# Kernel tuning notes

Measured on AMD Instinct MI355X. Metric: run time of the kernel, lower is better.

## Reference

```python
import jax, jax.numpy as jnp
import numpy as np

DEPTH, DIM, HEADS, DIM_HEAD, MLP = 6, 768, 12, 64, 3072
INNER = HEADS * DIM_HEAD  # 768
EPS = 1e-5


def _layernorm(x, w, b):
    m = jnp.mean(x, axis=-1, keepdims=True)
    v = jnp.mean((x - m) ** 2, axis=-1, keepdims=True)
    return (x - m) * jax.lax.rsqrt(v + EPS) * w + b


def setup_inputs() -> dict:
    key = jax.random.key(0)
    ks = jax.random.split(key, 12)
    s = 0.02
    return {
        "x": jax.random.normal(ks[0], (4, 1024, DIM), dtype=jnp.float32),
        "ln1_w": jnp.ones((DEPTH, DIM), jnp.float32),
        "ln1_b": jnp.zeros((DEPTH, DIM), jnp.float32),
        "w_qkv": jax.random.normal(ks[1], (DEPTH, DIM, 3 * INNER), jnp.float32) * s,
        "w_o": jax.random.normal(ks[2], (DEPTH, INNER, DIM), jnp.float32) * s,
        "b_o": jnp.zeros((DEPTH, DIM), jnp.float32),
        "ln2_w": jnp.ones((DEPTH, DIM), jnp.float32),
        "ln2_b": jnp.zeros((DEPTH, DIM), jnp.float32),
        "w1": jax.random.normal(ks[3], (DEPTH, DIM, MLP), jnp.float32) * s,
        "b1": jnp.zeros((DEPTH, MLP), jnp.float32),
        "w2": jax.random.normal(ks[4], (DEPTH, MLP, DIM), jnp.float32) * s,
        "b2": jnp.zeros((DEPTH, DIM), jnp.float32),
    }


def _forward(x, ln1_w, ln1_b, w_qkv, w_o, b_o, ln2_w, ln2_b, w1, b1, w2, b2):
    scale = DIM_HEAD ** -0.5
    b, n, _ = x.shape

    def block(x, p):
        l1w, l1b, wqkv, wo, bo, l2w, l2b, W1, B1, W2, B2 = p
        # --- attention (pre-norm); dropout/droppath are identity in eval ---
        h = _layernorm(x, l1w, l1b)
        qkv = h @ wqkv                                   # [b, n, 3*inner]
        q, k, v = jnp.split(qkv, 3, axis=-1)
        q = q.reshape(b, n, HEADS, DIM_HEAD).transpose(0, 2, 1, 3)
        k = k.reshape(b, n, HEADS, DIM_HEAD).transpose(0, 2, 1, 3)
        v = v.reshape(b, n, HEADS, DIM_HEAD).transpose(0, 2, 1, 3)
        dots = jnp.einsum('bhid,bhjd->bhij', q, k) * scale   # [b, h, n, n]
        attn = jax.nn.softmax(dots, axis=-1)
        out = jnp.einsum('bhij,bhjd->bhid', attn, v)
        out = out.transpose(0, 2, 1, 3).reshape(b, n, INNER)
        x = x + out @ wo + bo
        # --- feed-forward (pre-norm), exact GELU like torch default ---
        h = _layernorm(x, l2w, l2b)
        x = x + jax.nn.gelu(h @ W1 + B1, approximate=False) @ W2 + B2
        return x, None

    x, _ = jax.lax.scan(block, x, (ln1_w, ln1_b, w_qkv, w_o, b_o,
                                   ln2_w, ln2_b, w1, b1, w2, b2))
    return x


def reference(x, ln1_w, ln1_b, w_qkv, w_o, b_o, ln2_w, ln2_b, w1, b1, w2, b2):
    return _forward(x, ln1_w, ln1_b, w_qkv, w_o, b_o, ln2_w, ln2_b, w1, b1, w2, b2)
```

## Files before the change

### kernel.cpp

```cpp
#include <hip/hip_runtime.h>
#include <cmath>
#include <cstdint>

typedef __bf16 bf16_t;
typedef __bf16 bf16x8 __attribute__((ext_vector_type(8)));
typedef __bf16 bf16x4 __attribute__((ext_vector_type(4)));
typedef float  f32x4  __attribute__((ext_vector_type(4)));

#define DEPTH 6
#define DIM   768
#define HEADS 12
#define DH    64
#define MLPD  3072
#define SEQ   1024
#define BATCH 4
#define MTOT  (BATCH*SEQ)
#define QKVN  2304

static __device__ __forceinline__ bf16x8 ld8(const bf16_t* p) {
    return *(const bf16x8*)p;
}

typedef const __attribute__((address_space(1))) unsigned int gas_u32;
typedef __attribute__((address_space(3))) unsigned int las_u32;
static __device__ __forceinline__ void gload16(const bf16_t* g, bf16_t* l) {
    __builtin_amdgcn_global_load_lds((gas_u32*)g, (las_u32*)l, 16, 0, 0);
}

__global__ __launch_bounds__(256) void tcvt_kernel(const float* __restrict__ in,
                                                   bf16_t* __restrict__ out,
                                                   int K, int N) {
    __shared__ float ts[32][33];
    int n0 = blockIdx.x * 32, k0 = blockIdx.y * 32;
    size_t base = (size_t)blockIdx.z * K * N;
    int tx = threadIdx.x & 31, ty = threadIdx.x >> 5;
    #pragma unroll
    for (int r = 0; r < 32; r += 8)
        ts[ty + r][tx] = in[base + (size_t)(k0 + ty + r) * N + n0 + tx];
    __syncthreads();
    #pragma unroll
    for (int r = 0; r < 32; r += 8)
        out[base + (size_t)(n0 + ty + r) * K + k0 + tx] = (bf16_t)ts[tx][ty + r];
}

__global__ __launch_bounds__(192) void lnr_kernel(const float* __restrict__ xin,
                                                  float* __restrict__ xout,
                                                  const float* __restrict__ P,
                                                  int nslices,
                                                  const float* __restrict__ bias,
                                                  const float* __restrict__ w,
                                                  const float* __restrict__ b,
                                                  bf16_t* __restrict__ h,
                                                  int writeLN) {
    int row = blockIdx.x, t = threadIdx.x;
    size_t r4 = (size_t)row * 192 + t;
    float4 v = ((const float4*)xin)[r4];
    if (nslices) {
        float4 bi = ((const float4*)bias)[t];
        v.x += bi.x; v.y += bi.y; v.z += bi.z; v.w += bi.w;
        for (int s = 0; s < nslices; s++) {
            float4 pv = ((const float4*)P)[(size_t)s * MTOT * 192 + r4];
            v.x += pv.x; v.y += pv.y; v.z += pv.z; v.w += pv.w;
        }
        ((float4*)xout)[r4] = v;
    }
    float s = v.x + v.y + v.z + v.w;
    float q = v.x * v.x + v.y * v.y + v.z * v.z + v.w * v.w;
    #pragma unroll
    for (int off = 32; off > 0; off >>= 1) {
        s += __shfl_down(s, off);
        q += __shfl_down(q, off);
    }
    __shared__ float ss[3], sq[3], stat[2];
    if ((t & 63) == 0) { ss[t >> 6] = s; sq[t >> 6] = q; }
    __syncthreads();
    if (t == 0) {
        float S = ss[0] + ss[1] + ss[2];
        float Q = sq[0] + sq[1] + sq[2];
        float mean = S * (1.0f / DIM);
        float var  = Q * (1.0f / DIM) - mean * mean;
        stat[0] = mean;
        stat[1] = rsqrtf(var + 1e-5f);
    }
    __syncthreads();
    if (writeLN) {
        float mean = stat[0], rstd = stat[1];
        float4 wv4 = ((const float4*)w)[t];
        float4 bv4 = ((const float4*)b)[t];
        bf16x4 o;
        o[0] = (bf16_t)((v.x - mean) * rstd * wv4.x + bv4.x);
        o[1] = (bf16_t)((v.y - mean) * rstd * wv4.y + bv4.y);
        o[2] = (bf16_t)((v.z - mean) * rstd * wv4.z + bv4.z);
        o[3] = (bf16_t)((v.w - mean) * rstd * wv4.w + bv4.w);
        *(bf16x4*)&h[(size_t)row * DIM + t * 4] = o;
    }
}

template <int EPI, int BN>
__global__ __launch_bounds__(256) void gemm_kernel(const bf16_t* __restrict__ A,
                                                   const bf16_t* __restrict__ Bt,
                                                   const float* __restrict__ bias,
                                                   bf16_t* __restrict__ Cb,
                                                   float* __restrict__ Cf,
                                                   bf16_t* __restrict__ Vt,
                                                   int N, int K, int klen) {
    constexpr int NJ = BN / 32;
    __shared__ __align__(16) bf16_t As[3][128 * 32];
    __shared__ __align__(16) bf16_t Bs[3][BN * 32];
    int t = threadIdx.x;
    int m0 = blockIdx.y * 128, n0 = blockIdx.x * BN;
    int kz = blockIdx.z;
    int kbeg = kz * klen;
    int lane = t & 63, l16 = lane & 15, quad = lane >> 4;
    int wv = t >> 6, wm = wv >> 1, wn = wv & 1;
    f32x4 acc[4][NJ] = {};

    int sr = lane >> 2;
    int sc = ((lane & 3) ^ ((lane >> 3) & 3)) * 8;
    const bf16_t* gA0 = A  + (size_t)(m0 + wv * 32 + sr) * K + sc;
    const bf16_t* gA1 = gA0 + (size_t)16 * K;
    const bf16_t* gB0 = Bt + (size_t)(n0 + wv * (BN == 128 ? 32 : 16) + sr) * K + sc;
    const bf16_t* gB1 = gB0 + (size_t)16 * K;
    bf16_t* lA0 = &As[0][(wv * 32) * 32];
    bf16_t* lA1 = &As[0][(wv * 32 + 16) * 32];
    bf16_t* lB0 = &Bs[0][(wv * (BN == 128 ? 32 : 16)) * 32];
    bf16_t* lB1 = &Bs[0][(wv * 32 + 16) * 32];
    constexpr int bufA = 128 * 32;
    constexpr int bufB = BN * 32;

    auto stage = [&](int buf, int k0) {
        gload16(gA0 + k0, lA0 + buf * bufA);
        gload16(gA1 + k0, lA1 + buf * bufA);
        gload16(gB0 + k0, lB0 + buf * bufB);
        if constexpr (BN == 128) gload16(gB1 + k0, lB1 + buf * bufB);
    };

    int nIt = klen >> 5;
    stage(0, kbeg);
    if (nIt > 1) stage(1, kbeg + 32);
    int posA = (quad ^ ((l16 >> 1) & 3)) * 8;

    for (int it = 0; it < nIt; it++) {
        if (it + 1 < nIt) {
            if constexpr (BN == 128) asm volatile("s_waitcnt vmcnt(4)" ::: "memory");
            else                     asm volatile("s_waitcnt vmcnt(3)" ::: "memory");
        } else {
            asm volatile("s_waitcnt vmcnt(0)" ::: "memory");
        }
        __builtin_amdgcn_s_barrier();
        asm volatile("" ::: "memory");
        if (it + 2 < nIt) stage((it + 2) % 3, kbeg + (it + 2) * 32);
        const bf16_t* as = As[it % 3];
        const bf16_t* bs = Bs[it % 3];
        bf16x8 af[4], bfr[NJ];
        #pragma unroll
        for (int i = 0; i < 4; i++)
            af[i] = ld8(&as[(wm * 64 + i * 16 + l16) * 32 + posA]);
        #pragma unroll
        for (int j = 0; j < NJ; j++)
            bfr[j] = ld8(&bs[(wn * (16 * NJ) + j * 16 + l16) * 32 + posA]);
        #pragma unroll
        for (int i = 0; i < 4; i++)
            #pragma unroll
            for (int j = 0; j < NJ; j++)
                acc[i][j] = __builtin_amdgcn_mfma_f32_16x16x32_bf16(af[i], bfr[j], acc[i][j], 0, 0, 0);
    }

    if constexpr (EPI == 0) {
        if (n0 >= 1536) {
            int b = m0 >> 10;
            #pragma unroll
            for (int i = 0; i < 4; i++) {
                int n = (m0 & 1023) + wm * 64 + i * 16 + quad * 4;
                #pragma unroll
                for (int j = 0; j < NJ; j++) {
                    int hc = n0 + wn * (16 * NJ) + j * 16 + l16 - 1536;
                    int hh = hc >> 6, d = hc & 63;
                    bf16x4 ov;
                    #pragma unroll
                    for (int r = 0; r < 4; r++) ov[r] = (bf16_t)acc[i][j][r];
                    *(bf16x4*)&Vt[(((size_t)b * HEADS + hh) * 64 + d) * SEQ + n] = ov;
                }
            }
            return;
        }
    }
    #pragma unroll
    for (int i = 0; i < 4; i++) {
        int grow = m0 + wm * 64 + i * 16 + quad * 4;
        #pragma unroll
        for (int j = 0; j < NJ; j++) {
            int gcol = n0 + wn * (16 * NJ) + j * 16 + l16;
            float bv = 0.0f;
            if constexpr (EPI == 1) bv = bias[gcol];
            #pragma unroll
            for (int r = 0; r < 4; r++) {
                size_t idx = (size_t)(grow + r) * N + gcol;
                float v = acc[i][j][r];
                if constexpr (EPI == 0) {
                    Cb[idx] = (bf16_t)v;
                } else if constexpr (EPI == 1) {
                    v += bv;
                    v = 0.5f * v * (1.0f + erff(v * 0.70710678118654752f));
                    Cb[idx] = (bf16_t)v;
                } else {
                    Cf[(size_t)kz * MTOT * N + idx] = v;
                }
            }
        }
    }
}

__global__ __launch_bounds__(256) void attn_kernel(const bf16_t* __restrict__ qkv,
                                                   const bf16_t* __restrict__ vt,
                                                   bf16_t* __restrict__ out) {
    int qt = blockIdx.x, h = blockIdx.y, b = blockIdx.z;
    int t = threadIdx.x;
    int wv = t >> 6, lane = t & 63, l16 = lane & 15, quad = lane >> 4;
    const float LOG2E = 1.44269504f;
    int qw0 = qt * 64 + wv * 16;

    __shared__ __align__(16) bf16_t Ks[2][64 * 64];
    __shared__ __align__(16) bf16_t Vs[2][64 * 64];
    __shared__ __align__(16) bf16_t Pa[4][16 * 72];
    bf16_t* P = Pa[wv];

    size_t bS = (size_t)b * SEQ;
    const bf16_t* qrow = qkv + (bS + qw0 + l16) * QKVN + h * 64;
    bf16x8 qf0 = ld8(qrow + quad * 8);
    bf16x8 qf1 = ld8(qrow + 32 + quad * 8);

    float m = -3e38f, l = 0.0f;
    f32x4 o[4] = {};

    const bf16_t* kbase = qkv + bS * QKVN + 768 + h * 64;
    const bf16_t* vbase = vt + ((size_t)(b * HEADS + h) * 64) * SEQ;

    int ar = lane >> 3;
    int ac = ((lane & 7) ^ ar) * 8;
    int i0 = wv * 2, i1 = wv * 2 + 1;
    const bf16_t* gK0 = kbase + (size_t)(i0 * 8 + ar) * QKVN + ac;
    const bf16_t* gK1 = kbase + (size_t)(i1 * 8 + ar) * QKVN + ac;
    const bf16_t* gV0 = vbase + (size_t)(i0 * 8 + ar) * SEQ + ac;
    const bf16_t* gV1 = vbase + (size_t)(i1 * 8 + ar) * SEQ + ac;

    auto stage = [&](int buf, int kb) {
        gload16(gK0 + (size_t)kb * QKVN, &Ks[buf][i0 * 8 * 64]);
        gload16(gK1 + (size_t)kb * QKVN, &Ks[buf][i1 * 8 * 64]);
        gload16(gV0 + kb, &Vs[buf][i0 * 8 * 64]);
        gload16(gV1 + kb, &Vs[buf][i1 * 8 * 64]);
    };

    stage(0, 0);
    int p0 = (quad ^ (l16 & 7)) * 8;
    int p1 = ((quad + 4) ^ (l16 & 7)) * 8;

    for (int it = 0; it < SEQ / 64; it++) {
        __syncthreads();
        if (it + 1 < SEQ / 64) stage((it + 1) & 1, (it + 1) * 64);
        const bf16_t* ks = Ks[it & 1];
        const bf16_t* vs = Vs[it & 1];

        f32x4 s[4];
        #pragma unroll
        for (int tt = 0; tt < 4; tt++) {
            const bf16_t* kr = &ks[(tt * 16 + l16) * 64];
            f32x4 z = {};
            z = __builtin_amdgcn_mfma_f32_16x16x32_bf16(ld8(kr + p0), qf0, z, 0, 0, 0);
            z = __builtin_amdgcn_mfma_f32_16x16x32_bf16(ld8(kr + p1), qf1, z, 0, 0, 0);
            s[tt] = z;
        }
        float mx = -3e38f;
        #pragma unroll
        for (int tt = 0; tt < 4; tt++)
            #pragma unroll
            for (int r = 0; r < 4; r++) {
                s[tt][r] *= 0.125f;
                mx = fmaxf(mx, s[tt][r]);
            }
        mx = fmaxf(mx, __shfl_xor(mx, 16));
        mx = fmaxf(mx, __shfl_xor(mx, 32));
        float mn = fmaxf(m, mx);
        float alpha = exp2f((m - mn) * LOG2E);
        m = mn;
        float nb = mn * LOG2E;
        float rs = 0.0f;
        #pragma unroll
        for (int tt = 0; tt < 4; tt++) {
            bf16x4 pkt;
            #pragma unroll
            for (int r = 0; r < 4; r++) {
                float p = exp2f(fmaf(s[tt][r], LOG2E, -nb));
                rs += p;
                pkt[r] = (bf16_t)p;
            }
            *(bf16x4*)&P[l16 * 72 + tt * 16 + quad * 4] = pkt;
        }
        l = l * alpha + rs;
        #pragma unroll
        for (int jt = 0; jt < 4; jt++) o[jt] *= alpha;
        asm volatile("s_waitcnt lgkmcnt(0)" ::: "memory");
        bf16x8 pf0 = ld8(&P[l16 * 72 + quad * 8]);
        bf16x8 pf1 = ld8(&P[l16 * 72 + 32 + quad * 8]);
        #pragma unroll
        for (int jt = 0; jt < 4; jt++) {
            const bf16_t* vr = &vs[(jt * 16 + l16) * 64];
            o[jt] = __builtin_amdgcn_mfma_f32_16x16x32_bf16(ld8(vr + p0), pf0, o[jt], 0, 0, 0);
            o[jt] = __builtin_amdgcn_mfma_f32_16x16x32_bf16(ld8(vr + p1), pf1, o[jt], 0, 0, 0);
        }
    }

    l += __shfl_xor(l, 16);
    l += __shfl_xor(l, 32);
    float inv = 1.0f / l;
    bf16_t* orow = out + (bS + qw0 + l16) * DIM + h * 64;
    #pragma unroll
    for (int jt = 0; jt < 4; jt++) {
        bf16x4 ov;
        #pragma unroll
        for (int r = 0; r < 4; r++) ov[r] = (bf16_t)(o[jt][r] * inv);
        *(bf16x4*)&orow[jt * 16 + quad * 4] = ov;
    }
}

extern "C" void kernel_launch(void* const* d_in, const int* in_sizes, int n_in,
                              void* d_out, int out_size, void* d_ws, size_t ws_size,
                              hipStream_t stream) {
    const float* x     = (const float*)d_in[0];
    const float* ln1_w = (const float*)d_in[1];
    const float* ln1_b = (const float*)d_in[2];
    const float* w_qkv = (const float*)d_in[3];
    const float* w_o   = (const float*)d_in[4];
    const float* b_o   = (const float*)d_in[5];
    const float* ln2_w = (const float*)d_in[6];
    const float* ln2_b = (const float*)d_in[7];
    const float* w1    = (const float*)d_in[8];
    const float* b1    = (const float*)d_in[9];
    const float* w2    = (const float*)d_in[10];
    const float* b2    = (const float*)d_in[11];
    float* out = (float*)d_out;

    char* ws = (char*)d_ws;
    size_t off = 0;
    auto alloc = [&](size_t bytes) -> char* {
        char* p = ws + off;
        off += (bytes + 255) & ~(size_t)255;
        return p;
    };
    bf16_t* wqkv_t = (bf16_t*)alloc((size_t)DEPTH * DIM * QKVN * 2);
    bf16_t* wo_t   = (bf16_t*)alloc((size_t)DEPTH * DIM * DIM * 2);
    bf16_t* w1_t   = (bf16_t*)alloc((size_t)DEPTH * DIM * MLPD * 2);
    bf16_t* w2_t   = (bf16_t*)alloc((size_t)DEPTH * MLPD * DIM * 2);
    bf16_t* hbuf   = (bf16_t*)alloc((size_t)MTOT * DIM * 2);
    bf16_t* qkvb   = (bf16_t*)alloc((size_t)MTOT * QKVN * 2);
    bf16_t* vtb    = (bf16_t*)alloc((size_t)BATCH * HEADS * 64 * SEQ * 2);
    bf16_t* aob    = (bf16_t*)alloc((size_t)MTOT * DIM * 2);
    bf16_t* midb   = (bf16_t*)alloc((size_t)MTOT * MLPD * 2);
    float*  Pm     = (float*)alloc((size_t)4 * MTOT * DIM * 4);
    float*  Pp     = Pm;
    if (off > ws_size) return;

    tcvt_kernel<<<dim3(QKVN / 32, DIM / 32, DEPTH), 256, 0, stream>>>(w_qkv, wqkv_t, DIM, QKVN);
    tcvt_kernel<<<dim3(DIM / 32,  DIM / 32, DEPTH), 256, 0, stream>>>(w_o,   wo_t,   DIM, DIM);
    tcvt_kernel<<<dim3(MLPD / 32, DIM / 32, DEPTH), 256, 0, stream>>>(w1,    w1_t,   DIM, MLPD);
    tcvt_kernel<<<dim3(DIM / 32, MLPD / 32, DEPTH), 256, 0, stream>>>(w2,    w2_t,   MLPD, DIM);

    hipMemcpyAsync(out, x, (size_t)MTOT * DIM * 4, hipMemcpyDeviceToDevice, stream);

    lnr_kernel<<<MTOT, 192, 0, stream>>>(out, out, nullptr, 0, nullptr,
                                         ln1_w, ln1_b, hbuf, 1);

    for (int L = 0; L < DEPTH; L++) {
        gemm_kernel<0, 64><<<dim3(QKVN / 64, MTOT / 128, 1), 256, 0, stream>>>(
            hbuf, wqkv_t + (size_t)L * DIM * QKVN, nullptr, qkvb, nullptr, vtb,
            QKVN, DIM, DIM);
        attn_kernel<<<dim3(SEQ / 64, HEADS, BATCH), 256, 0, stream>>>(qkvb, vtb, aob);
        gemm_kernel<2, 64><<<dim3(DIM / 64, MTOT / 128, 2), 256, 0, stream>>>(
            aob, wo_t + (size_t)L * DIM * DIM, nullptr, nullptr, Pp, nullptr,
            DIM, DIM, 384);
        lnr_kernel<<<MTOT, 192, 0, stream>>>(out, out, Pp, 2, b_o + L * DIM,
                                             ln2_w + L * DIM, ln2_b + L * DIM, hbuf, 1);
        gemm_kernel<1, 64><<<dim3(MLPD / 64, MTOT / 128, 1), 256, 0, stream>>>(
            hbuf, w1_t + (size_t)L * DIM * MLPD, b1 + L * MLPD, midb, nullptr, nullptr,
            MLPD, DIM, DIM);
        gemm_kernel<2, 128><<<dim3(DIM / 128, MTOT / 128, 4), 256, 0, stream>>>(
            midb, w2_t + (size_t)L * MLPD * DIM, nullptr, nullptr, Pm, nullptr,
            DIM, MLPD, 768);
        if (L < DEPTH - 1) {
            lnr_kernel<<<MTOT, 192, 0, stream>>>(out, out, Pm, 4, b2 + L * DIM,
                                                 ln1_w + (L + 1) * DIM,
                                                 ln1_b + (L + 1) * DIM, hbuf, 1);
        } else {
            lnr_kernel<<<MTOT, 192, 0, stream>>>(out, out, Pm, 4, b2 + L * DIM,
                                                 ln1_w, ln1_b, hbuf, 0);
        }
    }
}
```

Baseline: 1.388 ms.

## Add double-buffer GEMM variant, widen tiles, and raise MFMA priority in attention

Templates the GEMM on buffer count and adds a 2-stage variant that uses __syncthreads instead of explicit vmcnt waits. The QKV and out-projection GEMMs move to 128-wide N tiles, and those two plus the W2 GEMM use double buffering. The attention kernel raises wave priority around its MFMA blocks with s_setprio. This trades pipeline depth and grid size (fewer blocks) for lower LDS use and more work per tile, and it risks exposing load latency.

```diff
diff --git a/kernel.cpp b/kernel.cpp
--- a/kernel.cpp
+++ b/kernel.cpp
@@ -96,7 +96,7 @@
     }
 }
 
-template <int EPI, int BN>
+template <int EPI, int BN, int NBUF>
 __global__ __launch_bounds__(256) void gemm_kernel(const bf16_t* __restrict__ A,
                                                    const bf16_t* __restrict__ Bt,
                                                    const float* __restrict__ bias,
@@ -105,8 +105,8 @@
                                                    bf16_t* __restrict__ Vt,
                                                    int N, int K, int klen) {
     constexpr int NJ = BN / 32;
-    __shared__ __align__(16) bf16_t As[3][128 * 32];
-    __shared__ __align__(16) bf16_t Bs[3][BN * 32];
+    __shared__ __align__(16) bf16_t As[NBUF][128 * 32];
+    __shared__ __align__(16) bf16_t Bs[NBUF][BN * 32];
     int t = threadIdx.x;
     int m0 = blockIdx.y * 128, n0 = blockIdx.x * BN;
     int kz = blockIdx.z;
@@ -137,21 +137,29 @@
 
     int nIt = klen >> 5;
     stage(0, kbeg);
-    if (nIt > 1) stage(1, kbeg + 32);
+    if constexpr (NBUF == 3) { if (nIt > 1) stage(1, kbeg + 32); }
     int posA = (quad ^ ((l16 >> 1) & 3)) * 8;
 
     for (int it = 0; it < nIt; it++) {
-        if (it + 1 < nIt) {
-            if constexpr (BN == 128) asm volatile("s_waitcnt vmcnt(4)" ::: "memory");
-            else                     asm volatile("s_waitcnt vmcnt(3)" ::: "memory");
+        int cur;
+        if constexpr (NBUF == 2) {
+            __syncthreads();
+            if (it + 1 < nIt) stage((it + 1) & 1, kbeg + (it + 1) * 32);
+            cur = it & 1;
         } else {
-            asm volatile("s_waitcnt vmcnt(0)" ::: "memory");
-        }
-        __builtin_amdgcn_s_barrier();
-        asm volatile("" ::: "memory");
-        if (it + 2 < nIt) stage((it + 2) % 3, kbeg + (it + 2) * 32);
-        const bf16_t* as = As[it % 3];
-        const bf16_t* bs = Bs[it % 3];
+            if (it + 1 < nIt) {
+                if constexpr (BN == 128) asm volatile("s_waitcnt vmcnt(4)" ::: "memory");
+                else                     asm volatile("s_waitcnt vmcnt(3)" ::: "memory");
+            } else {
+                asm volatile("s_waitcnt vmcnt(0)" ::: "memory");
+            }
+            __builtin_amdgcn_s_barrier();
+            asm volatile("" ::: "memory");
+            if (it + 2 < nIt) stage((it + 2) % 3, kbeg + (it + 2) * 32);
+            cur = it % 3;
+        }
+        const bf16_t* as = As[cur];
+        const bf16_t* bs = Bs[cur];
         bf16x8 af[4], bfr[NJ];
         #pragma unroll
         for (int i = 0; i < 4; i++)
@@ -262,6 +270,7 @@
         const bf16_t* vs = Vs[it & 1];
 
         f32x4 s[4];
+        __builtin_amdgcn_s_setprio(1);
         #pragma unroll
         for (int tt = 0; tt < 4; tt++) {
             const bf16_t* kr = &ks[(tt * 16 + l16) * 64];
@@ -270,6 +279,7 @@
             z = __builtin_amdgcn_mfma_f32_16x16x32_bf16(ld8(kr + p1), qf1, z, 0, 0, 0);
             s[tt] = z;
         }
+        __builtin_amdgcn_s_setprio(0);
         float mx = -3e38f;
         #pragma unroll
         for (int tt = 0; tt < 4; tt++)
@@ -302,12 +312,14 @@
         asm volatile("s_waitcnt lgkmcnt(0)" ::: "memory");
         bf16x8 pf0 = ld8(&P[l16 * 72 + quad * 8]);
         bf16x8 pf1 = ld8(&P[l16 * 72 + 32 + quad * 8]);
+        __builtin_amdgcn_s_setprio(1);
         #pragma unroll
         for (int jt = 0; jt < 4; jt++) {
             const bf16_t* vr = &vs[(jt * 16 + l16) * 64];
             o[jt] = __builtin_amdgcn_mfma_f32_16x16x32_bf16(ld8(vr + p0), pf0, o[jt], 0, 0, 0);
             o[jt] = __builtin_amdgcn_mfma_f32_16x16x32_bf16(ld8(vr + p1), pf1, o[jt], 0, 0, 0);
         }
+        __builtin_amdgcn_s_setprio(0);
     }
 
     l += __shfl_xor(l, 16);
@@ -371,19 +383,19 @@
                                          ln1_w, ln1_b, hbuf, 1);
 
     for (int L = 0; L < DEPTH; L++) {
-        gemm_kernel<0, 64><<<dim3(QKVN / 64, MTOT / 128, 1), 256, 0, stream>>>(
+        gemm_kernel<0, 128, 2><<<dim3(QKVN / 128, MTOT / 128, 1), 256, 0, stream>>>(
             hbuf, wqkv_t + (size_t)L * DIM * QKVN, nullptr, qkvb, nullptr, vtb,
             QKVN, DIM, DIM);
         attn_kernel<<<dim3(SEQ / 64, HEADS, BATCH), 256, 0, stream>>>(qkvb, vtb, aob);
-        gemm_kernel<2, 64><<<dim3(DIM / 64, MTOT / 128, 2), 256, 0, stream>>>(
+        gemm_kernel<2, 128, 2><<<dim3(DIM / 128, MTOT / 128, 2), 256, 0, stream>>>(
             aob, wo_t + (size_t)L * DIM * DIM, nullptr, nullptr, Pp, nullptr,
             DIM, DIM, 384);
         lnr_kernel<<<MTOT, 192, 0, stream>>>(out, out, Pp, 2, b_o + L * DIM,
                                              ln2_w + L * DIM, ln2_b + L * DIM, hbuf, 1);
-        gemm_kernel<1, 64><<<dim3(MLPD / 64, MTOT / 128, 1), 256, 0, stream>>>(
+        gemm_kernel<1, 64, 3><<<dim3(MLPD / 64, MTOT / 128, 1), 256, 0, stream>>>(
             hbuf, w1_t + (size_t)L * DIM * MLPD, b1 + L * MLPD, midb, nullptr, nullptr,
             MLPD, DIM, DIM);
-        gemm_kernel<2, 128><<<dim3(DIM / 128, MTOT / 128, 4), 256, 0, stream>>>(
+        gemm_kernel<2, 128, 2><<<dim3(DIM / 128, MTOT / 128, 4), 256, 0, stream>>>(
             midb, w2_t + (size_t)L * MLPD * DIM, nullptr, nullptr, Pm, nullptr,
             DIM, MLPD, 768);
         if (L < DEPTH - 1) {
```

Measured after the change: 1.335 ms. -3.8%, faster.

## Switch GEMM to double-buffered LDS with per-shape specialized kernels

Applied to the files above, without the earlier changes.

Replaces the triple-buffered LDS pipeline and its explicit vmcnt waits with a simpler double buffer synchronized by __syncthreads. It also wraps the GEMM body in four kernels whose sizes are compile-time constants, and moves the projection partial buffer into the qkv buffer. Smaller LDS use may allow more resident blocks and constant shapes help the compiler, but the prefetch distance drops from two stages to one. The double buffer also loses the explicit wait on the prefetched stage, which could expose load latency or even break correctness unless __syncthreads implies vmcnt(0).

```diff
diff --git a/kernel.cpp b/kernel.cpp
--- a/kernel.cpp
+++ b/kernel.cpp
@@ -97,16 +97,16 @@
 }
 
 template <int EPI, int BN>
-__global__ __launch_bounds__(256) void gemm_kernel(const bf16_t* __restrict__ A,
-                                                   const bf16_t* __restrict__ Bt,
-                                                   const float* __restrict__ bias,
-                                                   bf16_t* __restrict__ Cb,
-                                                   float* __restrict__ Cf,
-                                                   bf16_t* __restrict__ Vt,
-                                                   int N, int K, int klen) {
+static __device__ __forceinline__ void gemm_body(const bf16_t* __restrict__ A,
+                                                 const bf16_t* __restrict__ Bt,
+                                                 const float* __restrict__ bias,
+                                                 bf16_t* __restrict__ Cb,
+                                                 float* __restrict__ Cf,
+                                                 bf16_t* __restrict__ Vt,
+                                                 int N, int K, int klen) {
     constexpr int NJ = BN / 32;
-    __shared__ __align__(16) bf16_t As[3][128 * 32];
-    __shared__ __align__(16) bf16_t Bs[3][BN * 32];
+    __shared__ __align__(16) bf16_t As[2][128 * 32];
+    __shared__ __align__(16) bf16_t Bs[2][BN * 32];
     int t = threadIdx.x;
     int m0 = blockIdx.y * 128, n0 = blockIdx.x * BN;
     int kz = blockIdx.z;
@@ -137,21 +137,13 @@
 
     int nIt = klen >> 5;
     stage(0, kbeg);
-    if (nIt > 1) stage(1, kbeg + 32);
     int posA = (quad ^ ((l16 >> 1) & 3)) * 8;
 
     for (int it = 0; it < nIt; it++) {
-        if (it + 1 < nIt) {
-            if constexpr (BN == 128) asm volatile("s_waitcnt vmcnt(4)" ::: "memory");
-            else                     asm volatile("s_waitcnt vmcnt(3)" ::: "memory");
-        } else {
-            asm volatile("s_waitcnt vmcnt(0)" ::: "memory");
-        }
-        __builtin_amdgcn_s_barrier();
-        asm volatile("" ::: "memory");
-        if (it + 2 < nIt) stage((it + 2) % 3, kbeg + (it + 2) * 32);
-        const bf16_t* as = As[it % 3];
-        const bf16_t* bs = Bs[it % 3];
+        __syncthreads();
+        if (it + 1 < nIt) stage((it + 1) & 1, kbeg + (it + 1) * 32);
+        const bf16_t* as = As[it & 1];
+        const bf16_t* bs = Bs[it & 1];
         bf16x8 af[4], bfr[NJ];
         #pragma unroll
         for (int i = 0; i < 4; i++)
@@ -211,6 +203,29 @@
     }
 }
 
+__global__ __launch_bounds__(256) void qkv_gemm(const bf16_t* __restrict__ A,
+                                                const bf16_t* __restrict__ Bt,
+                                                bf16_t* __restrict__ Cb,
+                                                bf16_t* __restrict__ Vt) {
+    gemm_body<0, 64>(A, Bt, nullptr, Cb, nullptr, Vt, QKVN, DIM, DIM);
+}
+__global__ __launch_bounds__(256) void proj_gemm(const bf16_t* __restrict__ A,
+                                                 const bf16_t* __restrict__ Bt,
+                                                 float* __restrict__ Cf) {
+    gemm_body<2, 64>(A, Bt, nullptr, nullptr, Cf, nullptr, DIM, DIM, 384);
+}
+__global__ __launch_bounds__(256) void mlp1_gemm(const bf16_t* __restrict__ A,
+                                                 const bf16_t* __restrict__ Bt,
+                                                 const float* __restrict__ bias,
+                                                 bf16_t* __restrict__ Cb) {
+    gemm_body<1, 64>(A, Bt, bias, Cb, nullptr, nullptr, MLPD, DIM, DIM);
+}
+__global__ __launch_bounds__(256) void mlp2_gemm(const bf16_t* __restrict__ A,
+                                                 const bf16_t* __restrict__ Bt,
+                                                 float* __restrict__ Cf) {
+    gemm_body<2, 128>(A, Bt, nullptr, nullptr, Cf, nullptr, DIM, MLPD, 768);
+}
+
 __global__ __launch_bounds__(256) void attn_kernel(const bf16_t* __restrict__ qkv,
                                                    const bf16_t* __restrict__ vt,
                                                    bf16_t* __restrict__ out) {
@@ -357,7 +372,7 @@
     bf16_t* aob    = (bf16_t*)alloc((size_t)MTOT * DIM * 2);
     bf16_t* midb   = (bf16_t*)alloc((size_t)MTOT * MLPD * 2);
     float*  Pm     = (float*)alloc((size_t)4 * MTOT * DIM * 4);
-    float*  Pp     = Pm;
+    float*  Pp     = (float*)qkvb;
     if (off > ws_size) return;
 
     tcvt_kernel<<<dim3(QKVN / 32, DIM / 32, DEPTH), 256, 0, stream>>>(w_qkv, wqkv_t, DIM, QKVN);
@@ -371,21 +386,17 @@
                                          ln1_w, ln1_b, hbuf, 1);
 
     for (int L = 0; L < DEPTH; L++) {
-        gemm_kernel<0, 64><<<dim3(QKVN / 64, MTOT / 128, 1), 256, 0, stream>>>(
-            hbuf, wqkv_t + (size_t)L * DIM * QKVN, nullptr, qkvb, nullptr, vtb,
-            QKVN, DIM, DIM);
+        qkv_gemm<<<dim3(QKVN / 64, MTOT / 128, 1), 256, 0, stream>>>(
+            hbuf, wqkv_t + (size_t)L * DIM * QKVN, qkvb, vtb);
         attn_kernel<<<dim3(SEQ / 64, HEADS, BATCH), 256, 0, stream>>>(qkvb, vtb, aob);
-        gemm_kernel<2, 64><<<dim3(DIM / 64, MTOT / 128, 2), 256, 0, stream>>>(
-            aob, wo_t + (size_t)L * DIM * DIM, nullptr, nullptr, Pp, nullptr,
-            DIM, DIM, 384);
+        proj_gemm<<<dim3(DIM / 64, MTOT / 128, 2), 256, 0, stream>>>(
+            aob, wo_t + (size_t)L * DIM * DIM, Pp);
         lnr_kernel<<<MTOT, 192, 0, stream>>>(out, out, Pp, 2, b_o + L * DIM,
                                              ln2_w + L * DIM, ln2_b + L * DIM, hbuf, 1);
-        gemm_kernel<1, 64><<<dim3(MLPD / 64, MTOT / 128, 1), 256, 0, stream>>>(
-            hbuf, w1_t + (size_t)L * DIM * MLPD, b1 + L * MLPD, midb, nullptr, nullptr,
-            MLPD, DIM, DIM);
-        gemm_kernel<2, 128><<<dim3(DIM / 128, MTOT / 128, 4), 256, 0, stream>>>(
-            midb, w2_t + (size_t)L * MLPD * DIM, nullptr, nullptr, Pm, nullptr,
-            DIM, MLPD, 768);
+        mlp1_gemm<<<dim3(MLPD / 64, MTOT / 128, 1), 256, 0, stream>>>(
+            hbuf, w1_t + (size_t)L * DIM * MLPD, b1 + L * MLPD, midb);
+        mlp2_gemm<<<dim3(DIM / 128, MTOT / 128, 4), 256, 0, stream>>>(
+            midb, w2_t + (size_t)L * MLPD * DIM, Pm);
         if (L < DEPTH - 1) {
             lnr_kernel<<<MTOT, 192, 0, stream>>>(out, out, Pm, 4, b2 + L * DIM,
                                                  ln1_w + (L + 1) * DIM,
```

After: 1.359 ms. -2.1%, faster.
